# Kernel tuning notes

Hardware: AMD Instinct MI355X
Metric: run time of the kernel (lower is better)

## Reference

```python
import jax, jax.numpy as jnp
import numpy as np

S_MIN = 0.01
S_MAX = 36500.0
SEQ_LEN = 128
BATCH = 65536


def setup_inputs() -> dict:
    key = jax.random.key(0)
    k1, k2 = jax.random.split(key)
    # elapsed days: nonnegative floats; ratings: integers 1..4 stored as float
    t = jax.random.uniform(k1, (SEQ_LEN, BATCH), dtype=jnp.float32) * 30.0
    rating = jax.random.randint(k2, (SEQ_LEN, BATCH), 1, 5).astype(jnp.float32)
    inputs = jnp.stack([t, rating], axis=-1)  # [S, B, 2]
    w = jnp.array([0.4, 0.6, 2.4, 5.8, 4.93, 0.94, 0.86, 0.01, 1.49,
                   0.14, 0.94, 2.18, 0.05, 0.34, 1.26, 0.29, 2.61],
                  dtype=jnp.float32)
    return {"inputs": inputs, "w": w}


def _first_step(X, w):
    # state is all-zeros only on the first step (clamp keeps s >= S_MIN after)
    rating = X[:, 1]
    ridx = jnp.clip(rating.astype(jnp.int32) - 1, 0, 3)
    valid = (rating >= 1) & (rating <= 4)
    new_s = jnp.where(valid, w[ridx], 1.0)
    new_d = jnp.clip(w[4] - w[5] * (rating - 3.0), 1.0, 10.0)
    new_s = jnp.clip(new_s, S_MIN, S_MAX)
    return jnp.stack([new_s, new_d], axis=1)  # [B, 2]


def _step(w, state, X):
    s, d = state[:, 0], state[:, 1]
    t, rating = X[:, 0], X[:, 1]
    # power forgetting curve: r = (1 + t / (9 s))^-1
    r = 1.0 / (1.0 + t / (9.0 * s))
    hard_penalty = jnp.where(rating == 2, w[15], 1.0)
    easy_bonus = jnp.where(rating == 4, w[16], 1.0)
    s_success = s * (1.0 + jnp.exp(w[8]) * (11.0 - d) * jnp.power(s, -w[9])
                     * (jnp.exp((1.0 - r) * w[10]) - 1.0)
                     * hard_penalty * easy_bonus)
    s_failure = jnp.minimum(
        w[11] * jnp.power(d, -w[12]) * (jnp.power(s + 1.0, w[13]) - 1.0)
        * jnp.exp((1.0 - r) * w[14]),
        s)
    new_s = jnp.where(rating > 1.0, s_success, s_failure)
    new_d = d - w[6] * (rating - 3.0)
    new_d = w[7] * w[4] + (1.0 - w[7]) * new_d  # mean reversion to w[4]
    new_d = jnp.clip(new_d, 1.0, 10.0)
    new_s = jnp.clip(new_s, S_MIN, S_MAX)
    new_state = jnp.stack([new_s, new_d], axis=1)
    return new_state, new_state


def reference(inputs, w):
    state0 = _first_step(inputs[0], w)  # [B, 2]
    final_state, rest = jax.lax.scan(lambda st, X: _step(w, st, X),
                                     state0, inputs[1:])
    outputs = jnp.concatenate([state0[None], rest], axis=0)  # [S, B, 2]
    return outputs, final_state
```

## Files before the change

kernel.cpp:

```cpp
#include <hip/hip_runtime.h>

#define BATCH_N 65536
#define SEQ_N   128

typedef float v2f __attribute__((ext_vector_type(2)));

__global__ __launch_bounds__(256, 1) void fsrs_kernel(
    const v2f* __restrict__ in,
    const float* __restrict__ w,
    v2f*       __restrict__ out)
{
    const int b = blockIdx.x * 256 + threadIdx.x;

    const float w0 = w[0], w1 = w[1], w2 = w[2], w3 = w[3];
    const float w4 = w[4], w5 = w[5], w6 = w[6], w7 = w[7];
    const float w9 = w[9], w11 = w[11], w12 = w[12], w13 = w[13];
    const float w15 = w[15], w16 = w[16];
    constexpr float LOG2E = 1.44269504088896340736f;
    const float w8l  = w[8]  * LOG2E;
    const float w10l = w[10] * LOG2E;
    const float w14l = w[14] * LOG2E;
    const float omw7   = 1.0f - w7;
    const float omw7w6 = omw7 * w6;
    const float dc0    = w7 * w4 + 3.0f * omw7w6;

    const v2f* ip = in  + b;
    v2f*       op = out + b;

    float s = 0.01f;
    float dpre = 1.0f;

    v2f rawA[16], rawB[16];
    float tA[16], dA[16], mA[16];
    float tB[16], dB[16], mB[16];

    auto loadC = [&](v2f* raw, int base) {
#pragma unroll
        for (int i = 0; i < 16; ++i) raw[i] = ip[(base + i) * BATCH_N];
    };

    auto preC = [&](const v2f* raw, float* T, float* D, float* M, int lo) {
#pragma unroll
        for (int i = 0; i < 16; ++i) {
            if (i < lo) continue;
            const float tt = raw[i].x, rating = raw[i].y;
            const float hb = (rating == 2.0f) ? w15
                           : ((rating == 4.0f) ? w16 : 1.0f);
            const float eh = (11.0f - dpre) * hb;
            const float m2 = w11 * __builtin_amdgcn_exp2f(
                                 -w12 * __builtin_amdgcn_logf(dpre));
            M[i] = (rating > 1.0f) ? eh : -m2;
            const float nd = __builtin_fmaf(omw7, dpre,
                              __builtin_fmaf(-omw7w6, rating, dc0));
            dpre = fminf(fmaxf(nd, 1.0f), 10.0f);
            T[i] = tt;
            D[i] = dpre;
        }
    };

    auto stepC = [&](const float* T, const float* D, const float* M,
                     int base, int lo) {
#pragma unroll
        for (int i = 0; i < 16; ++i) {
            if (i < lo) continue;
            const float tt = T[i], ms = M[i];
            const bool  sel = ms > 0.0f;
            const float q   = __builtin_fmaf(9.0f, s, tt);
            const float omr = tt * __builtin_amdgcn_rcpf(q);
            const float e   = __builtin_amdgcn_exp2f(omr * (sel ? w10l : w14l));
            const float ls  = __builtin_amdgcn_logf(sel ? s : (s + 1.0f));
            const float aa  = sel ? __builtin_fmaf(-w9, ls, w8l) : (w13 * ls);
            const float A   = __builtin_amdgcn_exp2f(aa);
            const float Af  = sel ? A          : (A - 1.0f);
            const float Ef  = sel ? (e - 1.0f) : e;
            const float m   = sel ? (ms * s)   : (-ms);
            const float P   = Af * Ef * m;
            const float su  = fminf(s + P, 36500.0f);
            const float fl  = fmaxf(fminf(P, s), 0.01f);
            s = sel ? su : fl;
            v2f o; o.x = s; o.y = D[i];
            __builtin_nontemporal_store(o, &op[(base + i) * BATCH_N]);
        }
    };

    loadC(rawA, 0);
    loadC(rawB, 16);

    const float t0 = rawA[0].x, r0 = rawA[0].y;
    {
        const float d0 = fminf(fmaxf(
            __builtin_fmaf(-w5, r0 - 3.0f, w4), 1.0f), 10.0f);
        dpre = d0;
        tA[0] = t0; dA[0] = d0; mA[0] = 1.0f;
    }
    preC(rawA, tA, dA, mA, 1);
    loadC(rawA, 32);

    {
        const float wsel = (r0 < 2.5f) ? ((r0 < 1.5f) ? w0 : w1)
                                       : ((r0 < 3.5f) ? w2 : w3);
        const float ns = (r0 >= 1.0f && r0 <= 4.0f) ? wsel : 1.0f;
        s = fminf(fmaxf(ns, 0.01f), 36500.0f);
        v2f o; o.x = s; o.y = dA[0];
        __builtin_nontemporal_store(o, &op[0]);
    }
    stepC(tA, dA, mA, 0, 1);
    preC(rawB, tB, dB, mB, 0);
    loadC(rawB, 48);

#pragma unroll 1
    for (int c = 0; c < 2; ++c) {
        stepC(tB, dB, mB, 16 + 32 * c, 0);
        preC(rawA, tA, dA, mA, 0);
        loadC(rawA, 64 + 32 * c);
        stepC(tA, dA, mA, 32 + 32 * c, 0);
        preC(rawB, tB, dB, mB, 0);
        loadC(rawB, 80 + 32 * c);
    }

    stepC(tB, dB, mB, 80, 0);
    preC(rawA, tA, dA, mA, 0);
    stepC(tA, dA, mA, 96, 0);
    preC(rawB, tB, dB, mB, 0);
    stepC(tB, dB, mB, 112, 0);

    {
        v2f o; o.x = s; o.y = dB[15];
        op[SEQ_N * BATCH_N] = o;
    }
}

extern "C" void kernel_launch(void* const* d_in, const int* in_sizes, int n_in,
                              void* d_out, int out_size, void* d_ws, size_t ws_size,
                              hipStream_t stream) {
    const v2f*   in = (const v2f*)d_in[0];
    const float* w  = (const float*)d_in[1];
    v2f* out = (v2f*)d_out;
    fsrs_kernel<<<BATCH_N / 256, 256, 0, stream>>>(in, w, out);
}
```

Before: 115.0 us.

## Process two batch columns per thread with 128-bit vector loads and stores

```diff
diff --git a/kernel.cpp b/kernel.cpp
--- a/kernel.cpp
+++ b/kernel.cpp
@@ -2,15 +2,18 @@
 
 #define BATCH_N 65536
 #define SEQ_N   128
+#define CH      8
+#define RB      (BATCH_N / 2)
 
 typedef float v2f __attribute__((ext_vector_type(2)));
+typedef float v4f __attribute__((ext_vector_type(4)));
 
-__global__ __launch_bounds__(256, 1) void fsrs_kernel(
-    const v2f* __restrict__ in,
+__global__ __launch_bounds__(128, 1) void fsrs_kernel(
+    const v4f* __restrict__ in,
     const float* __restrict__ w,
-    v2f*       __restrict__ out)
+    v4f*       __restrict__ out)
 {
-    const int b = blockIdx.x * 256 + threadIdx.x;
+    const int g = blockIdx.x * 128 + threadIdx.x;
 
     const float w0 = w[0], w1 = w[1], w2 = w[2], w3 = w[3];
     const float w4 = w[4], w5 = w[5], w6 = w[6], w7 = w[7];
@@ -24,117 +27,138 @@
     const float omw7w6 = omw7 * w6;
     const float dc0    = w7 * w4 + 3.0f * omw7w6;
 
-    const v2f* ip = in  + b;
-    v2f*       op = out + b;
+    const v4f* ip = in  + g;
+    v4f*       op = out + g;
 
-    float s = 0.01f;
-    float dpre = 1.0f;
+    float s0 = 0.01f, s1 = 0.01f;
+    float dp0 = 1.0f, dp1 = 1.0f;
 
-    v2f rawA[16], rawB[16];
-    float tA[16], dA[16], mA[16];
-    float tB[16], dB[16], mB[16];
+    v4f rawA[CH], rawB[CH];
+    v2f tA[CH], dA[CH], mA[CH];
+    v2f tB[CH], dB[CH], mB[CH];
 
-    auto loadC = [&](v2f* raw, int base) {
+    auto loadC = [&](v4f* raw, int base) {
 #pragma unroll
-        for (int i = 0; i < 16; ++i) raw[i] = ip[(base + i) * BATCH_N];
+        for (int i = 0; i < CH; ++i)
+            raw[i] = __builtin_nontemporal_load(&ip[(base + i) * RB]);
     };
 
-    auto preC = [&](const v2f* raw, float* T, float* D, float* M, int lo) {
+    auto preRow = [&](float rating, float& dpre, float& D, float& M) {
+        const float hb = (rating == 2.0f) ? w15
+                       : ((rating == 4.0f) ? w16 : 1.0f);
+        const float eh = (11.0f - dpre) * hb;
+        const float m2 = w11 * __builtin_amdgcn_exp2f(
+                             -w12 * __builtin_amdgcn_logf(dpre));
+        M = (rating > 1.0f) ? eh : -m2;
+        const float nd = __builtin_fmaf(omw7, dpre,
+                          __builtin_fmaf(-omw7w6, rating, dc0));
+        dpre = fminf(fmaxf(nd, 1.0f), 10.0f);
+        D = dpre;
+    };
+
+    auto preC = [&](const v4f* raw, v2f* T, v2f* D, v2f* M, int lo) {
 #pragma unroll
-        for (int i = 0; i < 16; ++i) {
+        for (int i = 0; i < CH; ++i) {
             if (i < lo) continue;
-            const float tt = raw[i].x, rating = raw[i].y;
-            const float hb = (rating == 2.0f) ? w15
-                           : ((rating == 4.0f) ? w16 : 1.0f);
-            const float eh = (11.0f - dpre) * hb;
-            const float m2 = w11 * __builtin_amdgcn_exp2f(
-                                 -w12 * __builtin_amdgcn_logf(dpre));
-            M[i] = (rating > 1.0f) ? eh : -m2;
-            const float nd = __builtin_fmaf(omw7, dpre,
-                              __builtin_fmaf(-omw7w6, rating, dc0));
-            dpre = fminf(fmaxf(nd, 1.0f), 10.0f);
-            T[i] = tt;
-            D[i] = dpre;
+            v2f t; t.x = raw[i].x; t.y = raw[i].z;
+            float Dx, Mx, Dy, My;
+            preRow(raw[i].y, dp0, Dx, Mx);
+            preRow(raw[i].w, dp1, Dy, My);
+            T[i] = t;
+            v2f d; d.x = Dx; d.y = Dy; D[i] = d;
+            v2f m; m.x = Mx; m.y = My; M[i] = m;
         }
     };
 
-    auto stepC = [&](const float* T, const float* D, const float* M,
+    auto stepRow = [&](float tt, float ms, float& s) {
+        const bool  sel = ms > 0.0f;
+        const float q   = __builtin_fmaf(9.0f, s, tt);
+        const float omr = tt * __builtin_amdgcn_rcpf(q);
+        const float e   = __builtin_amdgcn_exp2f(omr * (sel ? w10l : w14l));
+        const float ls  = __builtin_amdgcn_logf(sel ? s : (s + 1.0f));
+        const float aa  = sel ? __builtin_fmaf(-w9, ls, w8l) : (w13 * ls);
+        const float A   = __builtin_amdgcn_exp2f(aa);
+        const float Af  = sel ? A          : (A - 1.0f);
+        const float Ef  = sel ? (e - 1.0f) : e;
+        const float m   = sel ? (ms * s)   : (-ms);
+        const float P   = Af * Ef * m;
+        const float su  = fminf(s + P, 36500.0f);
+        const float fl  = fmaxf(fminf(P, s), 0.01f);
+        s = sel ? su : fl;
+    };
+
+    auto stepC = [&](const v2f* T, const v2f* D, const v2f* M,
                      int base, int lo) {
 #pragma unroll
-        for (int i = 0; i < 16; ++i) {
+        for (int i = 0; i < CH; ++i) {
             if (i < lo) continue;
-            const float tt = T[i], ms = M[i];
-            const bool  sel = ms > 0.0f;
-            const float q   = __builtin_fmaf(9.0f, s, tt);
-            const float omr = tt * __builtin_amdgcn_rcpf(q);
-            const float e   = __builtin_amdgcn_exp2f(omr * (sel ? w10l : w14l));
-            const float ls  = __builtin_amdgcn_logf(sel ? s : (s + 1.0f));
-            const float aa  = sel ? __builtin_fmaf(-w9, ls, w8l) : (w13 * ls);
-            const float A   = __builtin_amdgcn_exp2f(aa);
-            const float Af  = sel ? A          : (A - 1.0f);
-            const float Ef  = sel ? (e - 1.0f) : e;
-            const float m   = sel ? (ms * s)   : (-ms);
-            const float P   = Af * Ef * m;
-            const float su  = fminf(s + P, 36500.0f);
-            const float fl  = fmaxf(fminf(P, s), 0.01f);
-            s = sel ? su : fl;
-            v2f o; o.x = s; o.y = D[i];
-            __builtin_nontemporal_store(o, &op[(base + i) * BATCH_N]);
+            stepRow(T[i].x, M[i].x, s0);
+            stepRow(T[i].y, M[i].y, s1);
+            v4f o; o.x = s0; o.y = D[i].x; o.z = s1; o.w = D[i].y;
+            __builtin_nontemporal_store(o, &op[(base + i) * RB]);
         }
     };
 
     loadC(rawA, 0);
-    loadC(rawB, 16);
+    loadC(rawB, CH);
 
-    const float t0 = rawA[0].x, r0 = rawA[0].y;
+    const float r00 = rawA[0].y, r01 = rawA[0].w;
     {
-        const float d0 = fminf(fmaxf(
-            __builtin_fmaf(-w5, r0 - 3.0f, w4), 1.0f), 10.0f);
-        dpre = d0;
-        tA[0] = t0; dA[0] = d0; mA[0] = 1.0f;
+        const float d00 = fminf(fmaxf(
+            __builtin_fmaf(-w5, r00 - 3.0f, w4), 1.0f), 10.0f);
+        const float d01 = fminf(fmaxf(
+            __builtin_fmaf(-w5, r01 - 3.0f, w4), 1.0f), 10.0f);
+        dp0 = d00; dp1 = d01;
+        v2f t; t.x = rawA[0].x; t.y = rawA[0].z; tA[0] = t;
+        v2f d; d.x = d00; d.y = d01; dA[0] = d;
+        v2f m; m.x = 1.0f; m.y = 1.0f; mA[0] = m;
     }
     preC(rawA, tA, dA, mA, 1);
-    loadC(rawA, 32);
+    loadC(rawA, 2 * CH);
 
     {
-        const float wsel = (r0 < 2.5f) ? ((r0 < 1.5f) ? w0 : w1)
-                                       : ((r0 < 3.5f) ? w2 : w3);
-        const float ns = (r0 >= 1.0f && r0 <= 4.0f) ? wsel : 1.0f;
-        s = fminf(fmaxf(ns, 0.01f), 36500.0f);
-        v2f o; o.x = s; o.y = dA[0];
+        const float ws0 = (r00 < 2.5f) ? ((r00 < 1.5f) ? w0 : w1)
+                                       : ((r00 < 3.5f) ? w2 : w3);
+        const float ws1 = (r01 < 2.5f) ? ((r01 < 1.5f) ? w0 : w1)
+                                       : ((r01 < 3.5f) ? w2 : w3);
+        const float n0 = (r00 >= 1.0f && r00 <= 4.0f) ? ws0 : 1.0f;
+        const float n1 = (r01 >= 1.0f && r01 <= 4.0f) ? ws1 : 1.0f;
+        s0 = fminf(fmaxf(n0, 0.01f), 36500.0f);
+        s1 = fminf(fmaxf(n1, 0.01f), 36500.0f);
+        v4f o; o.x = s0; o.y = dA[0].x; o.z = s1; o.w = dA[0].y;
         __builtin_nontemporal_store(o, &op[0]);
     }
     stepC(tA, dA, mA, 0, 1);
     preC(rawB, tB, dB, mB, 0);
-    loadC(rawB, 48);
+    loadC(rawB, 3 * CH);
 
 #pragma unroll 1
-    for (int c = 0; c < 2; ++c) {
-        stepC(tB, dB, mB, 16 + 32 * c, 0);
+    for (int c = 0; c < 6; ++c) {
+        stepC(tB, dB, mB, CH * (2 * c + 1), 0);
         preC(rawA, tA, dA, mA, 0);
-        loadC(rawA, 64 + 32 * c);
-        stepC(tA, dA, mA, 32 + 32 * c, 0);
+        loadC(rawA, CH * (2 * c + 4));
+        stepC(tA, dA, mA, CH * (2 * c + 2), 0);
         preC(rawB, tB, dB, mB, 0);
-        loadC(rawB, 80 + 32 * c);
+        loadC(rawB, CH * (2 * c + 5));
     }
 
-    stepC(tB, dB, mB, 80, 0);
+    stepC(tB, dB, mB, 13 * CH, 0);
     preC(rawA, tA, dA, mA, 0);
-    stepC(tA, dA, mA, 96, 0);
+    stepC(tA, dA, mA, 14 * CH, 0);
     preC(rawB, tB, dB, mB, 0);
-    stepC(tB, dB, mB, 112, 0);
+    stepC(tB, dB, mB, 15 * CH, 0);
 
     {
-        v2f o; o.x = s; o.y = dB[15];
-        op[SEQ_N * BATCH_N] = o;
+        v4f o; o.x = s0; o.y = dB[CH - 1].x; o.z = s1; o.w = dB[CH - 1].y;
+        op[SEQ_N * RB] = o;
     }
 }
 
 extern "C" void kernel_launch(void* const* d_in, const int* in_sizes, int n_in,
                               void* d_out, int out_size, void* d_ws, size_t ws_size,
                               hipStream_t stream) {
-    const v2f*   in = (const v2f*)d_in[0];
+    const v4f*   in = (const v4f*)d_in[0];
     const float* w  = (const float*)d_in[1];
-    v2f* out = (v2f*)d_out;
-    fsrs_kernel<<<BATCH_N / 256, 256, 0, stream>>>(in, w, out);
+    v4f* out = (v4f*)d_out;
+    fsrs_kernel<<<RB / 128, 128, 0, stream>>>(in, w, out);
 }
```

New measurement: 131.9 us. +14.7%, slower.

## Interleave next-chunk loads with the serial recurrence steps in groups of four

Applied to the files above, without the earlier changes.

```diff
diff --git a/kernel.cpp b/kernel.cpp
--- a/kernel.cpp
+++ b/kernel.cpp
@@ -31,8 +31,8 @@
     float dpre = 1.0f;
 
     v2f rawA[16], rawB[16];
-    float tA[16], dA[16], mA[16];
-    float tB[16], dB[16], mB[16];
+    float tX[16], dX[16], mX[16];
+    float tY[16], dY[16], mY[16];
 
     auto loadC = [&](v2f* raw, int base) {
 #pragma unroll
@@ -58,74 +58,84 @@
         }
     };
 
-    auto stepC = [&](const float* T, const float* D, const float* M,
-                     int base, int lo) {
+    auto stepRow = [&](float tt, float ms, float dd, int row) {
+        const bool  sel = ms > 0.0f;
+        const float q   = __builtin_fmaf(9.0f, s, tt);
+        const float omr = tt * __builtin_amdgcn_rcpf(q);
+        const float e   = __builtin_amdgcn_exp2f(omr * (sel ? w10l : w14l));
+        const float ls  = __builtin_amdgcn_logf(sel ? s : (s + 1.0f));
+        const float aa  = sel ? __builtin_fmaf(-w9, ls, w8l) : (w13 * ls);
+        const float A   = __builtin_amdgcn_exp2f(aa);
+        const float Af  = sel ? A          : (A - 1.0f);
+        const float Ef  = sel ? (e - 1.0f) : e;
+        const float m   = sel ? (ms * s)   : (-ms);
+        const float P   = Af * Ef * m;
+        const float su  = fminf(s + P, 36500.0f);
+        const float fl  = fmaxf(fminf(P, s), 0.01f);
+        s = sel ? su : fl;
+        v2f o; o.x = s; o.y = dd;
+        __builtin_nontemporal_store(o, &op[row * BATCH_N]);
+    };
+
+    auto phase = [&](const float* T, const float* D, const float* M,
+                     int base, int lo, v2f* raw, int loadBase, bool doLoad) {
 #pragma unroll
-        for (int i = 0; i < 16; ++i) {
-            if (i < lo) continue;
-            const float tt = T[i], ms = M[i];
-            const bool  sel = ms > 0.0f;
-            const float q   = __builtin_fmaf(9.0f, s, tt);
-            const float omr = tt * __builtin_amdgcn_rcpf(q);
-            const float e   = __builtin_amdgcn_exp2f(omr * (sel ? w10l : w14l));
-            const float ls  = __builtin_amdgcn_logf(sel ? s : (s + 1.0f));
-            const float aa  = sel ? __builtin_fmaf(-w9, ls, w8l) : (w13 * ls);
-            const float A   = __builtin_amdgcn_exp2f(aa);
-            const float Af  = sel ? A          : (A - 1.0f);
-            const float Ef  = sel ? (e - 1.0f) : e;
-            const float m   = sel ? (ms * s)   : (-ms);
-            const float P   = Af * Ef * m;
-            const float su  = fminf(s + P, 36500.0f);
-            const float fl  = fmaxf(fminf(P, s), 0.01f);
-            s = sel ? su : fl;
-            v2f o; o.x = s; o.y = D[i];
-            __builtin_nontemporal_store(o, &op[(base + i) * BATCH_N]);
+        for (int q = 0; q < 4; ++q) {
+            if (doLoad) {
+#pragma unroll
+                for (int j = 0; j < 4; ++j)
+                    raw[4 * q + j] = ip[(loadBase + 4 * q + j) * BATCH_N];
+            }
+#pragma unroll
+            for (int j = 0; j < 4; ++j) {
+                const int i = 4 * q + j;
+                if (i < lo) continue;
+                stepRow(T[i], M[i], D[i], base + i);
+            }
         }
     };
 
     loadC(rawA, 0);
     loadC(rawB, 16);
 
-    const float t0 = rawA[0].x, r0 = rawA[0].y;
+    const float r0 = rawA[0].y;
     {
         const float d0 = fminf(fmaxf(
             __builtin_fmaf(-w5, r0 - 3.0f, w4), 1.0f), 10.0f);
         dpre = d0;
-        tA[0] = t0; dA[0] = d0; mA[0] = 1.0f;
+        tX[0] = rawA[0].x; dX[0] = d0; mX[0] = 1.0f;
     }
-    preC(rawA, tA, dA, mA, 1);
-    loadC(rawA, 32);
+    preC(rawA, tX, dX, mX, 1);
 
     {
         const float wsel = (r0 < 2.5f) ? ((r0 < 1.5f) ? w0 : w1)
                                        : ((r0 < 3.5f) ? w2 : w3);
         const float ns = (r0 >= 1.0f && r0 <= 4.0f) ? wsel : 1.0f;
         s = fminf(fmaxf(ns, 0.01f), 36500.0f);
-        v2f o; o.x = s; o.y = dA[0];
+        v2f o; o.x = s; o.y = dX[0];
         __builtin_nontemporal_store(o, &op[0]);
     }
-    stepC(tA, dA, mA, 0, 1);
-    preC(rawB, tB, dB, mB, 0);
-    loadC(rawB, 48);
+    phase(tX, dX, mX, 0, 1, rawA, 32, true);
+    preC(rawB, tY, dY, mY, 0);
+    phase(tY, dY, mY, 16, 0, rawB, 48, true);
 
 #pragma unroll 1
     for (int c = 0; c < 2; ++c) {
-        stepC(tB, dB, mB, 16 + 32 * c, 0);
-        preC(rawA, tA, dA, mA, 0);
-        loadC(rawA, 64 + 32 * c);
-        stepC(tA, dA, mA, 32 + 32 * c, 0);
-        preC(rawB, tB, dB, mB, 0);
-        loadC(rawB, 80 + 32 * c);
+        preC(rawA, tX, dX, mX, 0);
+        phase(tX, dX, mX, 32 * (c + 1), 0,
+              rawA, 32 * (c + 2), true);
+        preC(rawB, tY, dY, mY, 0);
+        phase(tY, dY, mY, 32 * (c + 1) + 16, 0,
+              rawB, 32 * (c + 2) + 16, true);
     }
 
-    stepC(tB, dB, mB, 80, 0);
-    preC(rawA, tA, dA, mA, 0);
-    stepC(tA, dA, mA, 96, 0);
-    preC(rawB, tB, dB, mB, 0);
-    stepC(tB, dB, mB, 112, 0);
+    preC(rawA, tX, dX, mX, 0);
+    phase(tX, dX, mX, 96, 0, rawA, 0, false);
+    preC(rawB, tY, dY, mY, 0);
+    phase(tY, dY, mY, 112, 0, rawB, 0, false);
 
     {
-        v2f o; o.x = s; o.y = dB[15];
+        v2f o; o.x = s; o.y = dY[15];
         op[SEQ_N * BATCH_N] = o;
     }
 }
```

Result: no change. 113.7 us (-1.2%).
